# Kernel tuning notes

Measured on AMD Instinct MI355X. Metric: run time of the kernel, lower is better.

## Reference

```python
import jax, jax.numpy as jnp
import numpy as np

HEAD_DIM = 128
MAX_TIMESCALE = 10000.0
MIN_TIMESCALE = 1.0


def _rope(x, pos):
    # x: [B, S, H, D], pos: [B, S]
    d = x.shape[-1]
    fraction = 2.0 * jnp.arange(0, d // 2, dtype=jnp.float32) / d
    timescale = MIN_TIMESCALE * (MAX_TIMESCALE / MIN_TIMESCALE) ** fraction  # [D/2]
    sinusoid = pos.astype(jnp.float32)[..., None, None] / timescale  # [B,S,1,D/2]
    sin, cos = jnp.sin(sinusoid), jnp.cos(sinusoid)
    xf = x.astype(jnp.float32)
    x1, x2 = jnp.split(xf, 2, axis=-1)
    return jnp.concatenate((x1 * cos - x2 * sin, x2 * cos + x1 * sin), axis=-1).astype(x.dtype)


def setup_inputs() -> dict:
    key = jax.random.key(0)
    ks = jax.random.split(key, 5)
    B, T, D, N, K, H = 2, 2048, 2048, 16, 4, HEAD_DIM
    s = 0.02
    X = jax.random.normal(ks[0], (B, T, D), dtype=jnp.float32)
    q_positions = jnp.broadcast_to(jnp.arange(T, dtype=jnp.int32), (B, T))
    Wq = jax.random.normal(ks[1], (D, N, H), dtype=jnp.float32) * s
    Wk = jax.random.normal(ks[2], (D, K, H), dtype=jnp.float32) * s
    Wv = jax.random.normal(ks[3], (D, K, H), dtype=jnp.float32) * s
    Wo = jax.random.normal(ks[4], (N, H, D), dtype=jnp.float32) * s
    return {"X": X, "q_positions": q_positions, "Wq": Wq, "Wk": Wk, "Wv": Wv, "Wo": Wo}


def reference(X, q_positions, Wq, Wk, Wv, Wo):
    B, T, D = X.shape
    N, K = Wq.shape[1], Wk.shape[1]
    groups = N // K
    # fused QKV projections (DenseGeneral, no bias)
    q = jnp.einsum('btd,dnh->btnh', X, Wq)  # [B,T,N,H]
    k = jnp.einsum('btd,dkh->btkh', X, Wk)  # [B,T,K,H]
    v = jnp.einsum('btd,dkh->btkh', X, Wv)  # [B,T,K,H]
    # RoPE (note: original uses q_positions sin/cos for both q and k in the no-cache path)
    q = _rope(q, q_positions)
    k = _rope(k, q_positions)
    # GQA: broadcast kv heads to query heads
    k = jnp.repeat(k, groups, axis=2)  # [B,T,N,H]
    v = jnp.repeat(v, groups, axis=2)
    # attention with scale=1.0 and causal masking
    scores = jnp.einsum('btnh,bsnh->bnts', q, k)  # [B,N,T,T]
    causal = jnp.tril(jnp.ones((T, T), dtype=bool))
    scores = jnp.where(causal, scores, jnp.finfo(scores.dtype).min)
    probs = jax.nn.softmax(scores, axis=-1)
    attn = jnp.einsum('bnts,bsnh->btnh', probs, v)  # [B,T,N,H]
    # output projection contracting (head, head_dim)
    out = jnp.einsum('btnh,nhd->btd', attn, Wo)
    return out.astype(X.dtype)
```

## Files before the change

### kernel.cpp

```cpp
#include <hip/hip_runtime.h>
#include <math.h>

#define DEVI static __device__ __forceinline__

using f16x8 = __attribute__((ext_vector_type(8))) _Float16;
using h16x2 = __attribute__((ext_vector_type(2))) __fp16;
using f32x4  = __attribute__((ext_vector_type(4))) float;
using f32x16 = __attribute__((ext_vector_type(16))) float;

constexpr int Bb = 2, Tt = 2048, Dd = 2048, NQ = 16, NK = 4, HD = 128;
constexpr int Mrows = Bb * Tt;
constexpr int QKVC  = NQ*HD + 2*NK*HD;
constexpr int KOFF  = NQ*HD;
constexpr int VOFF  = NQ*HD + NK*HD;

DEVI ushort f2h(float f) {
  _Float16 h = (_Float16)f;
  union { _Float16 h; ushort u; } v; v.h = h;
  return v.u;
}
DEVI float h2f(ushort u) {
  union { ushort u; _Float16 h; } v; v.u = u;
  return (float)v.h;
}

typedef const __attribute__((address_space(1))) unsigned* gp1;
typedef __attribute__((address_space(3))) unsigned* lp3;
DEVI void gload16(void* lds, const void* g) {
  __builtin_amdgcn_global_load_lds((gp1)g, (lp3)lds, 16, 0, 0);
}

__global__ void k_cvt(const float* __restrict__ x, ushort* __restrict__ o, int n4) {
  int i = blockIdx.x * blockDim.x + threadIdx.x;
  if (i >= n4) return;
  float4 v = ((const float4*)x)[i];
  ushort4 u;
  u.x = f2h(v.x); u.y = f2h(v.y); u.z = f2h(v.z); u.w = f2h(v.w);
  ((ushort4*)o)[i] = u;
}

__global__ void k_tconv(const float* __restrict__ in, ushort* __restrict__ out, int R, int C) {
  __shared__ float t[32][33];
  const int c0 = blockIdx.x * 32, r0 = blockIdx.y * 32;
  const int tx = threadIdx.x, ty = threadIdx.y;
#pragma unroll
  for (int i = 0; i < 32; i += 8)
    t[ty + i][tx] = in[(size_t)(r0 + ty + i) * C + (c0 + tx)];
  __syncthreads();
#pragma unroll
  for (int i = 0; i < 32; i += 8)
    out[(size_t)(c0 + ty + i) * R + (r0 + tx)] = f2h(t[tx][ty + i]);
}

DEVI void stv(float* p, float v)  { *p = v; }
DEVI void stv(ushort* p, float v) { *p = f2h(v); }

template <typename OT>
__launch_bounds__(256)
__global__ void k_gemm_bt(const ushort* __restrict__ A, const ushort* __restrict__ Bt,
                          OT* __restrict__ C, int M, int N, int Kd) {
  __shared__ char As[8192];
  __shared__ char Bs[8192];
  const int tid = threadIdx.x;
  const int l = tid & 63, w = tid >> 6;
  const int wr = w >> 1, wc = w & 1;
  const int lr = l & 15, lk = l >> 4;
  const size_t row0 = (size_t)blockIdx.y * 128, col0 = (size_t)blockIdx.x * 128;

  f32x4 acc[4][4];
#pragma unroll
  for (int i = 0; i < 4; ++i)
#pragma unroll
    for (int j = 0; j < 4; ++j) acc[i][j] = (f32x4){0.f, 0.f, 0.f, 0.f};

  const int c0i = tid, c1i = tid + 256;
  const int ra0 = c0i >> 2, sa0 = (c0i & 3) ^ ((ra0 >> 1) & 3);
  const int ra1 = c1i >> 2, sa1 = (c1i & 3) ^ ((ra1 >> 1) & 3);

  for (int kt = 0; kt < Kd; kt += 32) {
    if (kt) __syncthreads();
    gload16(As + c0i * 16, A + (row0 + ra0) * Kd + kt + sa0 * 8);
    gload16(As + c1i * 16, A + (row0 + ra1) * Kd + kt + sa1 * 8);
    gload16(Bs + c0i * 16, Bt + (col0 + ra0) * Kd + kt + sa0 * 8);
    gload16(Bs + c1i * 16, Bt + (col0 + ra1) * Kd + kt + sa1 * 8);
    __syncthreads();
    f16x8 af[4], bfr[4];
#pragma unroll
    for (int i = 0; i < 4; ++i) {
      int ra = wr * 64 + i * 16 + lr;
      af[i] = *(const f16x8*)(As + ra * 64 + ((lk ^ ((ra >> 1) & 3)) << 4));
      int rb = wc * 64 + i * 16 + lr;
      bfr[i] = *(const f16x8*)(Bs + rb * 64 + ((lk ^ ((rb >> 1) & 3)) << 4));
    }
#pragma unroll
    for (int i = 0; i < 4; ++i)
#pragma unroll
      for (int j = 0; j < 4; ++j)
        acc[i][j] = __builtin_amdgcn_mfma_f32_16x16x32_f16(af[i], bfr[j], acc[i][j], 0, 0, 0);
  }
#pragma unroll
  for (int i = 0; i < 4; ++i) {
    size_t r = row0 + wr * 64 + i * 16 + lk * 4;
#pragma unroll
    for (int j = 0; j < 4; ++j) {
      size_t cc = col0 + wc * 64 + j * 16 + lr;
#pragma unroll
      for (int rg = 0; rg < 4; ++rg) stv(&C[(r + rg) * N + cc], acc[i][j][rg]);
    }
  }
}

__global__ void k_rope_tab(const int* __restrict__ pos, float* __restrict__ tab) {
  int idx = blockIdx.x * blockDim.x + threadIdx.x;
  if (idx >= Mrows * 64) return;
  int m = idx >> 6, i = idx & 63;
  double a = (double)pos[m] * exp2(-0.20762050593045952 * (double)i);
  tab[idx * 2]     = (float)cos(a);
  tab[idx * 2 + 1] = (float)sin(a);
}

__global__ void k_rope(ushort* __restrict__ qkv, const float* __restrict__ tab) {
  int idx = blockIdx.x * blockDim.x + threadIdx.x;
  if (idx >= Mrows * 20 * 8) return;
  int chunk = idx & 7;
  int h20 = (idx >> 3) % 20;
  int m = idx / 160;
  int colbase = (h20 < 16) ? h20 * 128 : (KOFF + (h20 - 16) * 128);
  size_t base = (size_t)m * QKVC + colbase + chunk * 8;
  union { uint4 v; ushort s[8]; } A1, A2, O1, O2;
  A1.v = *(const uint4*)(qkv + base);
  A2.v = *(const uint4*)(qkv + base + 64);
  const float* tp = tab + ((size_t)m * 64 + chunk * 8) * 2;
#pragma unroll
  for (int j = 0; j < 8; ++j) {
    float c = tp[2 * j], s = tp[2 * j + 1];
    float x1 = h2f(A1.s[j]), x2 = h2f(A2.s[j]);
    O1.s[j] = f2h(x1 * c - x2 * s);
    O2.s[j] = f2h(x2 * c + x1 * s);
  }
  *(uint4*)(qkv + base) = O1.v;
  *(uint4*)(qkv + base + 64) = O2.v;
}

__global__ void k_vt(const ushort* __restrict__ qkv, ushort* __restrict__ vt) {
  __shared__ ushort t[32][33];
  const int bg = blockIdx.z, bq = bg >> 2, g = bg & 3;
  const int s0 = blockIdx.x * 32, h0 = blockIdx.y * 32;
  const int tx = threadIdx.x, ty = threadIdx.y;
#pragma unroll
  for (int i = 0; i < 32; i += 8)
    t[ty + i][tx] = qkv[(size_t)(bq * Tt + s0 + ty + i) * QKVC + VOFF + g * HD + h0 + tx];
  __syncthreads();
  const int sx = (tx & 3) | ((tx & 8) >> 1) | ((tx & 4) << 1) | (tx & 16);
#pragma unroll
  for (int i = 0; i < 32; i += 8)
    vt[((size_t)bg * HD + h0 + ty + i) * Tt + (s0 + sx)] = t[tx][ty + i];
}

__launch_bounds__(256, 2)
__global__ void k_flash(const ushort* __restrict__ qkv, const ushort* __restrict__ vt,
                        ushort* __restrict__ attn) {
  __shared__ char Ks[2][16384];
  __shared__ char Vs[2][16384];
  const int b = blockIdx.x;
  const int vv = b >> 8, u = b & 255;
  const int hid = u >> 3, p = u & 7;
  const int qt = vv ? p : (15 - p);
  const int bq = hid >> 4, n = hid & 15, g = n >> 2;
  const int tid = threadIdx.x, w = tid >> 6, l = tid & 63;
  const int q5 = l & 31, hi = l >> 5;
  const int t0 = qt * 128;
  const int qrow = t0 + w * 32;
  const int qglob = qrow + q5;

  f16x8 qf[8];
  {
    const size_t qb = ((size_t)(bq * Tt + qglob)) * QKVC + n * HD + hi * 8;
#pragma unroll
    for (int kc = 0; kc < 8; ++kc) qf[kc] = *(const f16x8*)(qkv + qb + kc * 16);
  }
  f32x16 O[4];
#pragma unroll
  for (int ht = 0; ht < 4; ++ht)
#pragma unroll
    for (int r = 0; r < 16; ++r) O[ht][r] = 0.f;
  float m = -INFINITY, lsum = 0.f;

  const size_t kgbase = (size_t)(bq * Tt) * QKVC + KOFF + g * HD;
  const size_t vgbase = (size_t)(bq * 4 + g) * HD * Tt;
  const int ntiles = 2 * qt + 2;

#define STAGE(buf, s0s)                                                               \
  {                                                                                   \
    _Pragma("unroll")                                                                 \
    for (int cc = 0; cc < 4; ++cc) {                                                  \
      int c = cc * 256 + tid;                                                         \
      int sK = c >> 4, gK = (c & 15) ^ (sK & 15);                                     \
      gload16(Ks[buf] + c * 16, qkv + kgbase + (size_t)((s0s) + sK) * QKVC + gK * 8); \
      int hV = c >> 3, gV = (c & 7) ^ (hV & 7);                                       \
      gload16(Vs[buf] + c * 16, vt + vgbase + (size_t)hV * Tt + (s0s) + gV * 8);      \
    }                                                                                 \
  }

  STAGE(0, 0);
  __syncthreads();

  for (int j = 0; j < ntiles; ++j) {
    const int cur = j & 1;
    if (j + 1 < ntiles) STAGE(cur ^ 1, (j + 1) * 64);
    const int s0 = j * 64;
    if (s0 <= qrow + 31) {
      f32x16 sc[2];
      __builtin_amdgcn_s_setprio(1);
#pragma unroll
      for (int st = 0; st < 2; ++st) {
        f32x16 a;
#pragma unroll
        for (int r = 0; r < 16; ++r) a[r] = 0.f;
        const int sl = st * 32 + q5;
        const int ssw = (sl & 15) << 4;
#pragma unroll
        for (int kc = 0; kc < 8; ++kc) {
          f16x8 kf = *(const f16x8*)(Ks[cur] + sl * 256 + (((kc * 32 + hi * 16)) ^ ssw));
          a = __builtin_amdgcn_mfma_f32_32x32x16_f16(kf, qf[kc], a, 0, 0, 0);
        }
        sc[st] = a;
      }
      __builtin_amdgcn_s_setprio(0);
      if (s0 + 63 > qrow) {
#pragma unroll
        for (int st = 0; st < 2; ++st)
#pragma unroll
          for (int r = 0; r < 16; ++r) {
            int sg = s0 + st * 32 + (r & 3) + 8 * (r >> 2) + 4 * hi;
            if (sg > qglob) sc[st][r] = -INFINITY;
          }
      }
      float pm = -INFINITY;
#pragma unroll
      for (int st = 0; st < 2; ++st)
#pragma unroll
        for (int r = 0; r < 16; ++r) pm = fmaxf(pm, sc[st][r]);
      pm = fmaxf(pm, __shfl_xor(pm, 32));
      const bool doresc = !__all(pm - m <= 8.0f);
      float scl = 1.f;
      if (doresc) { float mn = fmaxf(m, pm); scl = __expf(m - mn); m = mn; }
      float rs = 0.f;
#pragma unroll
      for (int st = 0; st < 2; ++st)
#pragma unroll
        for (int r = 0; r < 16; ++r) { sc[st][r] = __expf(sc[st][r] - m); rs += sc[st][r]; }
      rs += __shfl_xor(rs, 32);
      if (doresc) {
        float sr[16];
#pragma unroll
        for (int r = 0; r < 16; ++r) sr[r] = __shfl(scl, (r & 3) + 8 * (r >> 2) + 4 * hi);
#pragma unroll
        for (int ht = 0; ht < 4; ++ht)
#pragma unroll
          for (int r = 0; r < 16; ++r) O[ht][r] *= sr[r];
        lsum = lsum * scl + rs;
      } else {
        lsum += rs;
      }
      unsigned pw[2][8];
#pragma unroll
      for (int st = 0; st < 2; ++st)
#pragma unroll
        for (int i = 0; i < 8; ++i) {
          union { h16x2 h; unsigned u; } t;
          t.h = __builtin_amdgcn_cvt_pkrtz(sc[st][2 * i], sc[st][2 * i + 1]);
          pw[st][i] = t.u;
        }
      __builtin_amdgcn_s_setprio(1);
#pragma unroll
      for (int ht = 0; ht < 4; ++ht) {
        const int hrow = ht * 32 + q5;
        const int hsw = (hrow & 7) << 4;
#pragma unroll
        for (int cc = 0; cc < 4; ++cc) {
          const int st = cc >> 1, ch = cc & 1;
          union { unsigned u[4]; f16x8 v; } pa;
          pa.u[0] = pw[st][ch * 4 + 0];
          pa.u[1] = pw[st][ch * 4 + 1];
          pa.u[2] = pw[st][ch * 4 + 2];
          pa.u[3] = pw[st][ch * 4 + 3];
          f16x8 vf = *(const f16x8*)(Vs[cur] + hrow * 128 + (((cc * 2 + hi) << 4) ^ hsw));
          O[ht] = __builtin_amdgcn_mfma_f32_32x32x16_f16(pa.v, vf, O[ht], 0, 0, 0);
        }
      }
      __builtin_amdgcn_s_setprio(0);
    }
    __syncthreads();
  }
#undef STAGE
  float iv[16];
#pragma unroll
  for (int r = 0; r < 16; ++r) iv[r] = 1.f / __shfl(lsum, (r & 3) + 8 * (r >> 2) + 4 * hi);
#pragma unroll
  for (int ht = 0; ht < 4; ++ht)
#pragma unroll
    for (int r = 0; r < 16; ++r) {
      size_t orow = (size_t)(bq * Tt + qrow + (r & 3) + 8 * (r >> 2) + 4 * hi);
      attn[orow * 2048 + n * HD + ht * 32 + q5] = f2h(O[ht][r] * iv[r]);
    }
}

extern "C" void kernel_launch(void* const* d_in, const int* in_sizes, int n_in,
                              void* d_out, int out_size, void* d_ws, size_t ws_size,
                              hipStream_t stream) {
  const float* X  = (const float*)d_in[0];
  const int*   qp = (const int*)d_in[1];
  const float* Wq = (const float*)d_in[2];
  const float* Wk = (const float*)d_in[3];
  const float* Wv = (const float*)d_in[4];
  const float* Wo = (const float*)d_in[5];
  float* out = (float*)d_out;
  char* ws = (char*)d_ws;

  ushort* Xf    = (ushort*)(ws + 0);
  ushort* WqkvT = (ushort*)(ws + 16777216);
  ushort* WoT   = (ushort*)(ws + 29360128);
  ushort* QKV   = (ushort*)(ws + 37748736);
  ushort* VT    = (ushort*)(ws + 62914560);
  ushort* attn  = (ushort*)(ws + 67108864);
  float*  tab   = (float*)(ws + 83886080);

  dim3 tb(32, 8);
  k_cvt<<<(Mrows * Dd / 4 + 255) / 256, 256, 0, stream>>>(X, Xf, Mrows * Dd / 4);
  k_tconv<<<dim3(64, 64), tb, 0, stream>>>(Wq, WqkvT, Dd, NQ * HD);
  k_tconv<<<dim3(16, 64), tb, 0, stream>>>(Wk, WqkvT + (size_t)KOFF * Dd, Dd, NK * HD);
  k_tconv<<<dim3(16, 64), tb, 0, stream>>>(Wv, WqkvT + (size_t)VOFF * Dd, Dd, NK * HD);
  k_tconv<<<dim3(64, 64), tb, 0, stream>>>(Wo, WoT, NQ * HD, Dd);
  k_gemm_bt<ushort><<<dim3(QKVC / 128, Mrows / 128), 256, 0, stream>>>(
      Xf, WqkvT, QKV, Mrows, QKVC, Dd);
  k_rope_tab<<<(Mrows * 64 + 255) / 256, 256, 0, stream>>>(qp, tab);
  k_rope<<<(Mrows * 160 + 255) / 256, 256, 0, stream>>>(QKV, tab);
  k_vt<<<dim3(Tt / 32, HD / 32, Bb * NK), tb, 0, stream>>>(QKV, VT);
  k_flash<<<dim3(512), 256, 0, stream>>>(QKV, VT, attn);
  k_gemm_bt<float><<<dim3(Dd / 128, Mrows / 128), 256, 0, stream>>>(
      attn, WoT, out, Mrows, Dd, Dd);
}
```

Baseline: 219.0 us.

## Merge prep kernels, fold log2e into Q, and use exp2 softmax with tree reductions

Merges the X conversion and RoPE table kernels into one launch, the four weight-transpose launches into one, and the RoPE and V-transpose kernels into one, cutting the launch count from eleven to six. Q is pre-scaled by log2(e) during RoPE so the flash kernel can use exp2f directly, and the rescale threshold rises to 11 in log2 units. The per-row max and sum reductions are restructured as pairwise trees, and the cross-half sum shuffle moves out of the loop to a single step at the end. Pre-scaling Q in fp16 adds a small rounding risk.

```diff
diff --git a/kernel.cpp b/kernel.cpp
--- a/kernel.cpp
+++ b/kernel.cpp
@@ -30,19 +30,37 @@
   __builtin_amdgcn_global_load_lds((gp1)g, (lp3)lds, 16, 0, 0);
 }
 
-__global__ void k_cvt(const float* __restrict__ x, ushort* __restrict__ o, int n4) {
-  int i = blockIdx.x * blockDim.x + threadIdx.x;
-  if (i >= n4) return;
-  float4 v = ((const float4*)x)[i];
-  ushort4 u;
-  u.x = f2h(v.x); u.y = f2h(v.y); u.z = f2h(v.z); u.w = f2h(v.w);
-  ((ushort4*)o)[i] = u;
-}
-
-__global__ void k_tconv(const float* __restrict__ in, ushort* __restrict__ out, int R, int C) {
+__global__ void k_prep(const float* __restrict__ x, ushort* __restrict__ o,
+                       const int* __restrict__ pos, float* __restrict__ tab) {
+  int b = blockIdx.x;
+  if (b < 8192) {
+    int i = b * 256 + threadIdx.x;
+    float4 v = ((const float4*)x)[i];
+    ushort4 u;
+    u.x = f2h(v.x); u.y = f2h(v.y); u.z = f2h(v.z); u.w = f2h(v.w);
+    ((ushort4*)o)[i] = u;
+  } else {
+    int idx = (b - 8192) * 256 + threadIdx.x;
+    int m = idx >> 6, i = idx & 63;
+    double a = (double)pos[m] * exp2(-0.20762050593045952 * (double)i);
+    tab[idx * 2]     = (float)cos(a);
+    tab[idx * 2 + 1] = (float)sin(a);
+  }
+}
+
+__global__ void k_tconv_all(const float* __restrict__ Wq, const float* __restrict__ Wk,
+                            const float* __restrict__ Wv, const float* __restrict__ Wo,
+                            ushort* __restrict__ WqkvT, ushort* __restrict__ WoT) {
   __shared__ float t[32][33];
-  const int c0 = blockIdx.x * 32, r0 = blockIdx.y * 32;
-  const int tx = threadIdx.x, ty = threadIdx.y;
+  int b = blockIdx.x;
+  const float* in; ushort* out; int C, bx, by;
+  if (b < 4096)      { in = Wq; out = WqkvT;                      C = 2048; bx = b & 63; by = b >> 6; }
+  else if (b < 5120) { b -= 4096; in = Wk; out = WqkvT + (size_t)KOFF * Dd; C = 512;  bx = b & 15; by = b >> 4; }
+  else if (b < 6144) { b -= 5120; in = Wv; out = WqkvT + (size_t)VOFF * Dd; C = 512;  bx = b & 15; by = b >> 4; }
+  else               { b -= 6144; in = Wo; out = WoT;             C = 2048; bx = b & 63; by = b >> 6; }
+  const int R = 2048;
+  const int c0 = bx * 32, r0 = by * 32;
+  const int tx = threadIdx.x & 31, ty = threadIdx.x >> 5;
 #pragma unroll
   for (int i = 0; i < 32; i += 8)
     t[ty + i][tx] = in[(size_t)(r0 + ty + i) * C + (c0 + tx)];
@@ -110,51 +128,46 @@
   }
 }
 
-__global__ void k_rope_tab(const int* __restrict__ pos, float* __restrict__ tab) {
-  int idx = blockIdx.x * blockDim.x + threadIdx.x;
-  if (idx >= Mrows * 64) return;
-  int m = idx >> 6, i = idx & 63;
-  double a = (double)pos[m] * exp2(-0.20762050593045952 * (double)i);
-  tab[idx * 2]     = (float)cos(a);
-  tab[idx * 2 + 1] = (float)sin(a);
-}
-
-__global__ void k_rope(ushort* __restrict__ qkv, const float* __restrict__ tab) {
-  int idx = blockIdx.x * blockDim.x + threadIdx.x;
-  if (idx >= Mrows * 20 * 8) return;
-  int chunk = idx & 7;
-  int h20 = (idx >> 3) % 20;
-  int m = idx / 160;
-  int colbase = (h20 < 16) ? h20 * 128 : (KOFF + (h20 - 16) * 128);
-  size_t base = (size_t)m * QKVC + colbase + chunk * 8;
-  union { uint4 v; ushort s[8]; } A1, A2, O1, O2;
-  A1.v = *(const uint4*)(qkv + base);
-  A2.v = *(const uint4*)(qkv + base + 64);
-  const float* tp = tab + ((size_t)m * 64 + chunk * 8) * 2;
-#pragma unroll
-  for (int j = 0; j < 8; ++j) {
-    float c = tp[2 * j], s = tp[2 * j + 1];
-    float x1 = h2f(A1.s[j]), x2 = h2f(A2.s[j]);
-    O1.s[j] = f2h(x1 * c - x2 * s);
-    O2.s[j] = f2h(x2 * c + x1 * s);
-  }
-  *(uint4*)(qkv + base) = O1.v;
-  *(uint4*)(qkv + base + 64) = O2.v;
-}
-
-__global__ void k_vt(const ushort* __restrict__ qkv, ushort* __restrict__ vt) {
-  __shared__ ushort t[32][33];
-  const int bg = blockIdx.z, bq = bg >> 2, g = bg & 3;
-  const int s0 = blockIdx.x * 32, h0 = blockIdx.y * 32;
-  const int tx = threadIdx.x, ty = threadIdx.y;
-#pragma unroll
-  for (int i = 0; i < 32; i += 8)
-    t[ty + i][tx] = qkv[(size_t)(bq * Tt + s0 + ty + i) * QKVC + VOFF + g * HD + h0 + tx];
-  __syncthreads();
-  const int sx = (tx & 3) | ((tx & 8) >> 1) | ((tx & 4) << 1) | (tx & 16);
-#pragma unroll
-  for (int i = 0; i < 32; i += 8)
-    vt[((size_t)bg * HD + h0 + ty + i) * Tt + (s0 + sx)] = t[tx][ty + i];
+__global__ void k_ropevt(ushort* __restrict__ qkv, const float* __restrict__ tab,
+                         ushort* __restrict__ vt) {
+  int b = blockIdx.x;
+  if (b < 2560) {
+    int idx = b * 256 + threadIdx.x;
+    int chunk = idx & 7;
+    int h20 = (idx >> 3) % 20;
+    int m = idx / 160;
+    const float qs = (h20 < 16) ? 1.4426950408889634f : 1.0f;
+    int colbase = (h20 < 16) ? h20 * 128 : (KOFF + (h20 - 16) * 128);
+    size_t base = (size_t)m * QKVC + colbase + chunk * 8;
+    union { uint4 v; ushort s[8]; } A1, A2, O1, O2;
+    A1.v = *(const uint4*)(qkv + base);
+    A2.v = *(const uint4*)(qkv + base + 64);
+    const float* tp = tab + ((size_t)m * 64 + chunk * 8) * 2;
+#pragma unroll
+    for (int j = 0; j < 8; ++j) {
+      float c = tp[2 * j], s = tp[2 * j + 1];
+      float x1 = h2f(A1.s[j]), x2 = h2f(A2.s[j]);
+      O1.s[j] = f2h((x1 * c - x2 * s) * qs);
+      O2.s[j] = f2h((x2 * c + x1 * s) * qs);
+    }
+    *(uint4*)(qkv + base) = O1.v;
+    *(uint4*)(qkv + base + 64) = O2.v;
+  } else {
+    __shared__ ushort t[32][33];
+    b -= 2560;
+    const int x = b & 63, y = (b >> 6) & 3, bg = b >> 8;
+    const int bq = bg >> 2, g = bg & 3;
+    const int s0 = x * 32, h0 = y * 32;
+    const int tx = threadIdx.x & 31, ty = threadIdx.x >> 5;
+#pragma unroll
+    for (int i = 0; i < 32; i += 8)
+      t[ty + i][tx] = qkv[(size_t)(bq * Tt + s0 + ty + i) * QKVC + VOFF + g * HD + h0 + tx];
+    __syncthreads();
+    const int sx = (tx & 3) | ((tx & 8) >> 1) | ((tx & 4) << 1) | (tx & 16);
+#pragma unroll
+    for (int i = 0; i < 32; i += 8)
+      vt[((size_t)bg * HD + h0 + ty + i) * Tt + (s0 + sx)] = t[tx][ty + i];
+  }
 }
 
 __launch_bounds__(256, 2)
@@ -167,10 +180,9 @@
   const int hid = u >> 3, p = u & 7;
   const int qt = vv ? p : (15 - p);
   const int bq = hid >> 4, n = hid & 15, g = n >> 2;
-  const int tid = threadIdx.x, w = tid >> 6, l = tid & 63;
+  const int tid = threadIdx.x, l = tid & 63, w = tid >> 6;
   const int q5 = l & 31, hi = l >> 5;
-  const int t0 = qt * 128;
-  const int qrow = t0 + w * 32;
+  const int qrow = qt * 128 + w * 32;
   const int qglob = qrow + q5;
 
   f16x8 qf[8];
@@ -236,21 +248,31 @@
             if (sg > qglob) sc[st][r] = -INFINITY;
           }
       }
-      float pm = -INFINITY;
+      float tm[16];
+#pragma unroll
+      for (int r = 0; r < 16; ++r) tm[r] = fmaxf(sc[0][r], sc[1][r]);
+#pragma unroll
+      for (int d = 8; d > 0; d >>= 1)
+#pragma unroll
+        for (int i = 0; i < 8; ++i)
+          if (i < d) tm[i] = fmaxf(tm[i], tm[i + d]);
+      float pm = fmaxf(tm[0], __shfl_xor(tm[0], 32));
+      const bool doresc = !__all(pm - m <= 11.0f);
+      float scl = 1.f;
+      if (doresc) { float mn = fmaxf(m, pm); scl = exp2f(m - mn); m = mn; }
 #pragma unroll
       for (int st = 0; st < 2; ++st)
 #pragma unroll
-        for (int r = 0; r < 16; ++r) pm = fmaxf(pm, sc[st][r]);
-      pm = fmaxf(pm, __shfl_xor(pm, 32));
-      const bool doresc = !__all(pm - m <= 8.0f);
-      float scl = 1.f;
-      if (doresc) { float mn = fmaxf(m, pm); scl = __expf(m - mn); m = mn; }
-      float rs = 0.f;
-#pragma unroll
-      for (int st = 0; st < 2; ++st)
-#pragma unroll
-        for (int r = 0; r < 16; ++r) { sc[st][r] = __expf(sc[st][r] - m); rs += sc[st][r]; }
-      rs += __shfl_xor(rs, 32);
+        for (int r = 0; r < 16; ++r) sc[st][r] = exp2f(sc[st][r] - m);
+      float ts[16];
+#pragma unroll
+      for (int r = 0; r < 16; ++r) ts[r] = sc[0][r] + sc[1][r];
+#pragma unroll
+      for (int d = 8; d > 0; d >>= 1)
+#pragma unroll
+        for (int i = 0; i < 8; ++i)
+          if (i < d) ts[i] += ts[i + d];
+      const float rs = ts[0];
       if (doresc) {
         float sr[16];
 #pragma unroll
@@ -279,12 +301,11 @@
         const int hsw = (hrow & 7) << 4;
 #pragma unroll
         for (int cc = 0; cc < 4; ++cc) {
-          const int st = cc >> 1, ch = cc & 1;
-          union { unsigned u[4]; f16x8 v; } pa;
-          pa.u[0] = pw[st][ch * 4 + 0];
-          pa.u[1] = pw[st][ch * 4 + 1];
-          pa.u[2] = pw[st][ch * 4 + 2];
-          pa.u[3] = pw[st][ch * 4 + 3];
+          union { unsigned uu[4]; f16x8 v; } pa;
+          pa.uu[0] = pw[cc >> 1][(cc & 1) * 4 + 0];
+          pa.uu[1] = pw[cc >> 1][(cc & 1) * 4 + 1];
+          pa.uu[2] = pw[cc >> 1][(cc & 1) * 4 + 2];
+          pa.uu[3] = pw[cc >> 1][(cc & 1) * 4 + 3];
           f16x8 vf = *(const f16x8*)(Vs[cur] + hrow * 128 + (((cc * 2 + hi) << 4) ^ hsw));
           O[ht] = __builtin_amdgcn_mfma_f32_32x32x16_f16(pa.v, vf, O[ht], 0, 0, 0);
         }
@@ -294,9 +315,10 @@
     __syncthreads();
   }
 #undef STAGE
+  const float ltot = lsum + __shfl_xor(lsum, 32);
   float iv[16];
 #pragma unroll
-  for (int r = 0; r < 16; ++r) iv[r] = 1.f / __shfl(lsum, (r & 3) + 8 * (r >> 2) + 4 * hi);
+  for (int r = 0; r < 16; ++r) iv[r] = 1.f / __shfl(ltot, (r & 3) + 8 * (r >> 2) + 4 * hi);
 #pragma unroll
   for (int ht = 0; ht < 4; ++ht)
 #pragma unroll
@@ -326,17 +348,11 @@
   ushort* attn  = (ushort*)(ws + 67108864);
   float*  tab   = (float*)(ws + 83886080);
 
-  dim3 tb(32, 8);
-  k_cvt<<<(Mrows * Dd / 4 + 255) / 256, 256, 0, stream>>>(X, Xf, Mrows * Dd / 4);
-  k_tconv<<<dim3(64, 64), tb, 0, stream>>>(Wq, WqkvT, Dd, NQ * HD);
-  k_tconv<<<dim3(16, 64), tb, 0, stream>>>(Wk, WqkvT + (size_t)KOFF * Dd, Dd, NK * HD);
-  k_tconv<<<dim3(16, 64), tb, 0, stream>>>(Wv, WqkvT + (size_t)VOFF * Dd, Dd, NK * HD);
-  k_tconv<<<dim3(64, 64), tb, 0, stream>>>(Wo, WoT, NQ * HD, Dd);
+  k_prep<<<9216, 256, 0, stream>>>(X, Xf, qp, tab);
+  k_tconv_all<<<10240, 256, 0, stream>>>(Wq, Wk, Wv, Wo, WqkvT, WoT);
   k_gemm_bt<ushort><<<dim3(QKVC / 128, Mrows / 128), 256, 0, stream>>>(
       Xf, WqkvT, QKV, Mrows, QKVC, Dd);
-  k_rope_tab<<<(Mrows * 64 + 255) / 256, 256, 0, stream>>>(qp, tab);
-  k_rope<<<(Mrows * 160 + 255) / 256, 256, 0, stream>>>(QKV, tab);
-  k_vt<<<dim3(Tt / 32, HD / 32, Bb * NK), tb, 0, stream>>>(QKV, VT);
+  k_ropevt<<<4608, 256, 0, stream>>>(QKV, tab, VT);
   k_flash<<<dim3(512), 256, 0, stream>>>(QKV, VT, attn);
   k_gemm_bt<float><<<dim3(Dd / 128, Mrows / 128), 256, 0, stream>>>(
       attn, WoT, out, Mrows, Dd, Dd);
```

After: 222.5 us. About the same (+1.6%).
